# Performance work log

Measured on AMD Instinct MI355X. Metric: run time of the kernel, lower is better.

## Reference

```python
import jax, jax.numpy as jnp
import numpy as np

COMMITMENT_COST = 0.25


def setup_inputs() -> dict:
    key = jax.random.key(0)
    k1, k2 = jax.random.split(key)
    z_e = jax.random.normal(k1, (8, 2048, 768), dtype=jnp.float32)
    # torch init is uniform(-1/K, 1/K); scale is irrelevant for correctness,
    # but match it for realism.
    K = 8192
    embedding = jax.random.uniform(k2, (K, 768), dtype=jnp.float32,
                                   minval=-1.0 / K, maxval=1.0 / K)
    return {"z_e": z_e, "embedding": embedding}


def reference(z_e, embedding):
    """VectorQuantizer.forward (eval mode: no EMA side effects).

    Returns (quantized_st, indices, loss) exactly as the torch module.
    """
    B, S, D = z_e.shape
    flat = z_e.reshape(-1, D)  # [N, D]
    distances = (jnp.sum(flat * flat, axis=1, keepdims=True)
                 + jnp.sum(embedding * embedding, axis=1)
                 - 2.0 * flat @ embedding.T)
    indices = jnp.argmin(distances, axis=1)          # [N]
    quantized = embedding[indices].reshape(B, S, D)  # codebook lookup
    indices = indices.reshape(B, S)
    # commitment loss: mse(stop_grad(quantized), z_e)
    e_latent_loss = jnp.mean((jax.lax.stop_gradient(quantized) - z_e) ** 2)
    loss = COMMITMENT_COST * e_latent_loss
    # straight-through estimator
    quantized_st = z_e + jax.lax.stop_gradient(quantized - z_e)
    return quantized_st, indices, loss
```

## Files before the change

### kernel.cpp

```cpp
#include <hip/hip_runtime.h>
#include <cfloat>

#define NROWS 16384
#define DIM   768
#define KC    8192
#define MARGIN 2.5e-4f
#define NBLK_EMIT (NROWS / 4)

#define BM 256
#define BN 256
#define BK 32
#define NKT (DIM / BK)
#define NCB (KC / BN)

#define NBLK_ZCVT (NROWS / 4)
#define NBLK_ECVT (KC * DIM / 8 / 256)

typedef unsigned short ushort_t;
typedef __attribute__((ext_vector_type(8))) short short8v;
typedef __attribute__((ext_vector_type(4))) float f32x4;

__device__ __forceinline__ ushort_t f2bf(float f) {
  unsigned u = __float_as_uint(f);
  return (ushort_t)((u + 0x7FFFu + ((u >> 16) & 1u)) >> 16);
}

__device__ __forceinline__ void gload_lds16(const void* g, void* l) {
  using GP = const __attribute__((address_space(1))) void*;
  using LP = __attribute__((address_space(3))) void*;
  GP gp = (GP)(unsigned long long)(uintptr_t)g;
  LP lp = (LP)(unsigned)(uintptr_t)l;
  __builtin_amdgcn_global_load_lds(gp, lp, 16, 0, 0);
}

__global__ __launch_bounds__(256)
void cvt_all_kernel(const float* __restrict__ z, ushort_t* __restrict__ zh,
                    float* __restrict__ x2, const float* __restrict__ emb,
                    ushort_t* __restrict__ eh) {
#pragma clang fp contract(off)
  if (blockIdx.x < NBLK_ZCVT) {
    const int w    = threadIdx.x >> 6;
    const int lane = threadIdx.x & 63;
    const int n    = blockIdx.x * 4 + w;
    const float* zr = z + (size_t)n * DIM;

    {
      const float4* zg = (const float4*)zr;
      uint2* zo = (uint2*)(zh + (size_t)n * DIM);
      #pragma unroll
      for (int i = 0; i < 3; ++i) {
        const float4 f = zg[lane + 64 * i];
        uint2 o;
        o.x = (unsigned)f2bf(f.x) | ((unsigned)f2bf(f.y) << 16);
        o.y = (unsigned)f2bf(f.z) | ((unsigned)f2bf(f.w) << 16);
        zo[lane + 64 * i] = o;
      }
    }

    const int chunk = lane >> 3;
    const int j     = lane & 7;
    const float* p  = zr + chunk * 96 + j;
    float v0 = p[0];
    float r  = v0 * v0;
    #pragma unroll
    for (int k = 1; k < 12; ++k) {
      const float v  = p[8 * k];
      const float sq = v * v;
      r = r + sq;
    }
    r = r + __shfl_xor(r, 1);
    r = r + __shfl_xor(r, 2);
    r = r + __shfl_xor(r, 4);
    r = r + __shfl_xor(r, 8);
    r = r + __shfl_xor(r, 16);
    r = r + __shfl_xor(r, 32);
    if (lane == 0) x2[n] = r;
  } else {
    const int i = (blockIdx.x - NBLK_ZCVT) * 256 + threadIdx.x;
    const float4* s4 = (const float4*)emb;
    const float4 f0 = s4[2 * i], f1 = s4[2 * i + 1];
    uint4 o;
    o.x = (unsigned)f2bf(f0.x) | ((unsigned)f2bf(f0.y) << 16);
    o.y = (unsigned)f2bf(f0.z) | ((unsigned)f2bf(f0.w) << 16);
    o.z = (unsigned)f2bf(f1.x) | ((unsigned)f2bf(f1.y) << 16);
    o.w = (unsigned)f2bf(f1.z) | ((unsigned)f2bf(f1.w) << 16);
    ((uint4*)eh)[i] = o;
  }
}

__global__ __launch_bounds__(512, 2)
void gemm5(const ushort_t* __restrict__ zh, const ushort_t* __restrict__ eh,
           float4* __restrict__ subtop) {
  __shared__ __align__(16) ushort_t Ash[3][BM * BK];
  __shared__ __align__(16) ushort_t Bsh[3][BN * BK];
  __shared__ float4 ltop[BM][4];

  const int t    = threadIdx.x;
  const int w    = t >> 6, lane = t & 63;
  const int wr   = w >> 2;
  const int wcn  = w & 3;
  const int row0 = blockIdx.y * BM;
  const int col0 = blockIdx.x * BN;

  const int srow  = w * 32 + (lane >> 2);
  const int sslot = lane & 3;
  const ushort_t* zsA[2];
  const ushort_t* esB[2];
  #pragma unroll
  for (int q = 0; q < 2; ++q) {
    const int r = srow + q * 16;
    const int j = sslot ^ ((r >> 1) & 3);
    zsA[q] = zh + (size_t)(row0 + r) * DIM + j * 8;
    esB[q] = eh + (size_t)(col0 + r) * DIM + j * 8;
  }

#define STAGE_A_S(ktv, SLOT) do {                                         \
    _Pragma("unroll")                                                     \
    for (int q = 0; q < 2; ++q)                                           \
      gload_lds16(zsA[q] + (ktv) * 32, &Ash[SLOT][w * 1024 + q * 512]);   \
  } while (0)
#define STAGE_B_S(ktv, SLOT) do {                                         \
    _Pragma("unroll")                                                     \
    for (int q = 0; q < 2; ++q)                                           \
      gload_lds16(esB[q] + (ktv) * 32, &Bsh[SLOT][w * 1024 + q * 512]);   \
  } while (0)

  f32x4 acc[8][4];
  #pragma unroll
  for (int m = 0; m < 8; ++m)
    #pragma unroll
    for (int n = 0; n < 4; ++n) acc[m][n] = (f32x4){0.f, 0.f, 0.f, 0.f};

  STAGE_A_S(0, 0); STAGE_B_S(0, 0);
  STAGE_A_S(1, 1); STAGE_B_S(1, 1);
  asm volatile("s_waitcnt vmcnt(4)" ::: "memory");
  __builtin_amdgcn_s_barrier();
  __builtin_amdgcn_sched_barrier(0);

#define TILE_STEP(ktv, RB, RS) do {                                           \
    short8v bfr[4], afr[8];                                                   \
      \
    _Pragma("unroll")                                                         \
    for (int n = 0; n < 4; ++n) {                                             \
      const int c  = wcn * 64 + n * 16 + (lane & 15);                         \
      const int sl = (lane >> 4) ^ ((c >> 1) & 3);                            \
      bfr[n] = *(const short8v*)&Bsh[RB][c * 32 + sl * 8];                    \
    }                                                                         \
    _Pragma("unroll")                                                         \
    for (int m = 0; m < 8; ++m) {                                             \
      const int r  = wr * 128 + m * 16 + (lane & 15);                         \
      const int sl = (lane >> 4) ^ ((r >> 1) & 3);                            \
      afr[m] = *(const short8v*)&Ash[RB][r * 32 + sl * 8];                    \
    }                                                                         \
    if ((ktv) + 2 < NKT) { STAGE_A_S((ktv) + 2, RS); STAGE_B_S((ktv) + 2, RS); } \
    _Pragma("unroll")                                                         \
    for (int m = 0; m < 8; ++m)                                               \
      _Pragma("unroll")                                                       \
      for (int n = 0; n < 4; ++n)                                             \
        acc[m][n] = __builtin_amdgcn_mfma_f32_16x16x32_bf16(afr[m], bfr[n],   \
                                                            acc[m][n], 0, 0, 0); \
       \
    asm volatile("s_waitcnt lgkmcnt(0)" ::: "memory");                        \
    if ((ktv) < NKT - 2) asm volatile("s_waitcnt vmcnt(4)" ::: "memory");     \
    else                 asm volatile("s_waitcnt vmcnt(0)" ::: "memory");     \
    __builtin_amdgcn_s_barrier();                                             \
    asm volatile("" ::: "memory");                                            \
    __builtin_amdgcn_sched_barrier(0);                                        \
  } while (0)

  #pragma unroll 1
  for (int u = 0; u < NKT / 3; ++u) {
    const int kt = u * 3;
    TILE_STEP(kt + 0, 0, 2);
    TILE_STEP(kt + 1, 1, 0);
    TILE_STEP(kt + 2, 2, 1);
  }
#undef TILE_STEP
#undef STAGE_A_S
#undef STAGE_B_S

  __syncthreads();
  #pragma unroll
  for (int m = 0; m < 8; ++m) {
    #pragma unroll
    for (int reg = 0; reg < 4; ++reg) {
      float v1 = FLT_MAX, v2 = FLT_MAX; int i1 = 0, i2 = 0;
      #pragma unroll
      for (int n = 0; n < 4; ++n) {
        const float v = -2.0f * acc[m][n][reg];
        const int   c = col0 + wcn * 64 + n * 16 + (lane & 15);
        if (v < v1)      { v2 = v1; i2 = i1; v1 = v; i1 = c; }
        else if (v < v2) { v2 = v; i2 = c; }
      }
      #pragma unroll
      for (int off = 1; off < 16; off <<= 1) {
        const float ov1 = __shfl_xor(v1, off); const int oi1 = __shfl_xor(i1, off);
        const float ov2 = __shfl_xor(v2, off); const int oi2 = __shfl_xor(i2, off);
        if (ov1 < v1) {
          const float nv2 = (v1 < ov2) ? v1 : ov2;
          const int   ni2 = (v1 < ov2) ? i1 : oi2;
          v1 = ov1; i1 = oi1; v2 = nv2; i2 = ni2;
        } else if (ov1 < v2) { v2 = ov1; i2 = oi1; }
      }
      const int rloc = wr * 128 + m * 16 + (lane >> 4) * 4 + reg;
      if ((lane & 15) == 0)
        ltop[rloc][wcn] = make_float4(v1, __int_as_float(i1), v2, __int_as_float(i2));
    }
  }
  __syncthreads();
  if (t < BM) {
    float v1 = FLT_MAX, v2 = FLT_MAX; int i1 = 0x7fffffff, i2 = 0x7fffffff;
    #pragma unroll
    for (int g = 0; g < 4; ++g) {
      const float4 P = ltop[t][g];
      const float pv1 = P.x; const int pi1 = __float_as_int(P.y);
      const float pv2 = P.z; const int pi2 = __float_as_int(P.w);
      if (pv1 < v1)      { v2 = v1; i2 = i1; v1 = pv1; i1 = pi1; }
      else if (pv1 < v2) { v2 = pv1; i2 = pi1; }
      if (pv2 < v1)      { v2 = v1; i2 = i1; v1 = pv2; i1 = pi2; }
      else if (pv2 < v2) { v2 = pv2; i2 = pi2; }
    }
    subtop[(size_t)(row0 + t) * NCB + blockIdx.x] =
        make_float4(v1, __int_as_float(i1), v2, __int_as_float(i2));
  }
}

__global__ __launch_bounds__(256)
void selemit_k(const float* __restrict__ z, const float* __restrict__ emb,
               const float* __restrict__ x2, const float4* __restrict__ subtop,
               float* __restrict__ out, double* __restrict__ partials) {
  __shared__ float zbuf[4][DIM];
  __shared__ float ebufA[4][DIM];
  __shared__ float ebufB[4][DIM];
  __shared__ double wsum[4];

  const int w    = threadIdx.x >> 6;
  const int lane = threadIdx.x & 63;
  const int n    = blockIdx.x * 4 + w;

  float v1 = FLT_MAX, v2 = FLT_MAX;
  int i1 = 0x7fffffff;
  if (lane < NCB) {
    const float4 e = subtop[(size_t)n * NCB + lane];
    v1 = e.x; i1 = __float_as_int(e.y);
    v2 = e.z;
  }

  float rowmin = v1;
  #pragma unroll
  for (int off = 32; off; off >>= 1) rowmin = fminf(rowmin, __shfl_xor(rowmin, off));
  const float thr = rowmin + MARGIN;

  const unsigned long long mA = __ballot(v1 <= thr);
  const unsigned long long mB = __ballot(v2 <= thr);

  int winner;
  if (mB == 0 && __popcll(mA) == 1) {
    winner = __shfl(i1, __builtin_ctzll(mA));
  } else {
    const float x2n = x2[n];
    {
      const float4* zg = (const float4*)(z + (size_t)n * DIM);
      float4* zl = (float4*)zbuf[w];
      #pragma unroll
      for (int i = 0; i < 3; ++i) zl[lane + 64 * i] = zg[lane + 64 * i];
    }
    float bd = FLT_MAX; int bc = 0x7fffffff;

    unsigned long long mS = mA & ~mB;
    while (mS) {
      const int s0 = __builtin_ctzll(mS); mS &= mS - 1;
      int s1 = -1;
      if (mS) { s1 = __builtin_ctzll(mS); mS &= mS - 1; }
      const int ca = __shfl(i1, s0);
      const int cb = (s1 >= 0) ? __shfl(i1, s1) : -1;
      {
        const float4* eg = (const float4*)(emb + (size_t)ca * DIM);
        float4* el = (float4*)ebufA[w];
        #pragma unroll
        for (int i = 0; i < 3; ++i) el[lane + 64 * i] = eg[lane + 64 * i];
      }
      if (cb >= 0) {
        const float4* eg = (const float4*)(emb + (size_t)cb * DIM);
        float4* el = (float4*)ebufB[w];
        #pragma unroll
        for (int i = 0; i < 3; ++i) el[lane + 64 * i] = eg[lane + 64 * i];
      }
      asm volatile("s_waitcnt lgkmcnt(0)" ::: "memory");
      const float4* zl4 = (const float4*)zbuf[w];
      const float4* la4 = (const float4*)ebufA[w];
      const float4* lb4 = (const float4*)ebufB[w];
      float da = 0.f, db = 0.f;
      #pragma unroll 8
      for (int kq = 0; kq < DIM / 4; ++kq) {
        const float4 zz = zl4[kq];
        const float4 aa = la4[kq];
        const float4 bb = lb4[kq];
        da = fmaf(zz.x, aa.x, da); db = fmaf(zz.x, bb.x, db);
        da = fmaf(zz.y, aa.y, da); db = fmaf(zz.y, bb.y, db);
        da = fmaf(zz.z, aa.z, da); db = fmaf(zz.z, bb.z, db);
        da = fmaf(zz.w, aa.w, da); db = fmaf(zz.w, bb.w, db);
      }
      const float sa = x2n - 2.0f * da;
      if (sa < bd || (sa == bd && ca < bc)) { bd = sa; bc = ca; }
      if (cb >= 0) {
        const float sb = x2n - 2.0f * db;
        if (sb < bd || (sb == bd && cb < bc)) { bd = sb; bc = cb; }
      }
    }

    unsigned long long m = mB;
    if (m) {
      const float* zr = z + (size_t)n * DIM;
      float bdL = FLT_MAX; int bcL = 0x7fffffff;
      while (m) {
        const int s = __builtin_ctzll(m); m &= m - 1;
        const int c0 = s * BN + lane;
        const float* p0 = emb + (size_t)c0 * DIM;
        const float* p1 = p0 + (size_t)64 * DIM;
        const float* p2 = p0 + (size_t)128 * DIM;
        const float* p3 = p0 + (size_t)192 * DIM;
        float d0 = 0.f, d1 = 0.f, d2 = 0.f, d3 = 0.f;
        #pragma unroll 4
        for (int k = 0; k < DIM; ++k) {
          const float zk = zr[k];
          d0 = fmaf(zk, p0[k], d0);
          d1 = fmaf(zk, p1[k], d1);
          d2 = fmaf(zk, p2[k], d2);
          d3 = fmaf(zk, p3[k], d3);
        }
        const float s0 = x2n - 2.0f * d0;
        const float s1 = x2n - 2.0f * d1;
        const float s2 = x2n - 2.0f * d2;
        const float s3 = x2n - 2.0f * d3;
        if (s0 < bdL || (s0 == bdL && c0 < bcL))       { bdL = s0; bcL = c0; }
        if (s1 < bdL || (s1 == bdL && c0 + 64 < bcL))  { bdL = s1; bcL = c0 + 64; }
        if (s2 < bdL || (s2 == bdL && c0 + 128 < bcL)) { bdL = s2; bcL = c0 + 128; }
        if (s3 < bdL || (s3 == bdL && c0 + 192 < bcL)) { bdL = s3; bcL = c0 + 192; }
      }
      #pragma unroll
      for (int off = 32; off; off >>= 1) {
        const float ov = __shfl_xor(bdL, off);
        const int   oc = __shfl_xor(bcL, off);
        if (ov < bdL || (ov == bdL && oc < bcL)) { bdL = ov; bcL = oc; }
      }
      if (bdL < bd || (bdL == bd && bcL < bc)) { bd = bdL; bc = bcL; }
    }
    winner = bc;
  }

  const float4* zr4 = (const float4*)(z + (size_t)n * DIM);
  const float4* er4 = (const float4*)(emb + (size_t)winner * DIM);
  float4* outr = (float4*)(out + (size_t)n * DIM);
  double lsum = 0.0;
  #pragma unroll
  for (int i = 0; i < 3; ++i) {
    const int idx = lane + 64 * i;
    const float4 zz = zr4[idx];
    const float4 qq = er4[idx];
    float4 o;
    o.x = zz.x + (qq.x - zz.x); o.y = zz.y + (qq.y - zz.y);
    o.z = zz.z + (qq.z - zz.z); o.w = zz.w + (qq.w - zz.w);
    outr[idx] = o;
    const float dx = qq.x - zz.x, dy = qq.y - zz.y;
    const float dz = qq.z - zz.z, dw = qq.w - zz.w;
    lsum = fma((double)dx, (double)dx, lsum);
    lsum = fma((double)dy, (double)dy, lsum);
    lsum = fma((double)dz, (double)dz, lsum);
    lsum = fma((double)dw, (double)dw, lsum);
  }
  #pragma unroll
  for (int off = 32; off; off >>= 1) lsum += __shfl_xor(lsum, off);
  if (lane == 0) {
    out[(size_t)NROWS * DIM + n] = (float)winner;
    wsum[w] = lsum;
  }
  __syncthreads();
  if (threadIdx.x == 0)
    partials[blockIdx.x] = ((wsum[0] + wsum[1]) + (wsum[2] + wsum[3]));
}

__global__ __launch_bounds__(256)
void fin_kernel(const double* __restrict__ partials, float* __restrict__ out) {
  __shared__ double red[256];
  const int t = threadIdx.x;
  double s = 0.0;
  #pragma unroll
  for (int i = 0; i < NBLK_EMIT / 256; ++i) s += partials[t * (NBLK_EMIT / 256) + i];
  red[t] = s;
  __syncthreads();
  for (int off = 128; off; off >>= 1) {
    if (t < off) red[t] += red[t + off];
    __syncthreads();
  }
  if (t == 0)
    out[(size_t)NROWS * DIM + NROWS] =
        (float)(0.25 * red[0] / (double)((size_t)NROWS * DIM));
}

extern "C" void kernel_launch(void* const* d_in, const int* in_sizes, int n_in,
                              void* d_out, int out_size, void* d_ws, size_t ws_size,
                              hipStream_t stream) {
  const float* z   = (const float*)d_in[0];
  const float* emb = (const float*)d_in[1];
  float* out = (float*)d_out;
  char*  ws  = (char*)d_ws;

  double*   partials = (double*)ws;
  float*    x2       = (float*)(ws + 32768);
  ushort_t* zh       = (ushort_t*)(ws + 163840);
  ushort_t* eh       = (ushort_t*)(ws + 25329664);
  float4*   subtop   = (float4*)(ws + 37912576);

  cvt_all_kernel<<<NBLK_ZCVT + NBLK_ECVT, 256, 0, stream>>>(z, zh, x2, emb, eh);
  gemm5<<<dim3(KC / BN, NROWS / BM), 512, 0, stream>>>(zh, eh, subtop);
  selemit_k<<<NROWS / 4, 256, 0, stream>>>(z, emb, x2, subtop, out, partials);
  fin_kernel<<<1, 256, 0, stream>>>(partials, out);
}
```

Baseline: 462.3 us.

## Shrink GEMM column tile to 128 and alias top-2 scratch onto LDS

Halves the codebook tile width (BN 256→128) so each 8-wave block computes a 256x128 tile with 4x4 MFMA accumulators per wave instead of 8x4. The aim is lower register pressure, higher occupancy and more blocks in the grid. The per-row top-2 scratch now reuses the A-tile LDS buffer instead of a separate array. The refine kernel is adjusted to 64 column-block candidates per row, which fills every lane. The cost is less operand reuse per loaded tile and twice as much subtop data written and read.

```diff
diff --git a/kernel.cpp b/kernel.cpp
--- a/kernel.cpp
+++ b/kernel.cpp
@@ -8,7 +8,7 @@
 #define NBLK_EMIT (NROWS / 4)
 
 #define BM 256
-#define BN 256
+#define BN 128
 #define BK 32
 #define NKT (DIM / BK)
 #define NCB (KC / BN)
@@ -88,80 +88,67 @@
   }
 }
 
-__global__ __launch_bounds__(512, 2)
-void gemm5(const ushort_t* __restrict__ zh, const ushort_t* __restrict__ eh,
+__global__ __launch_bounds__(512)
+void gemm6(const ushort_t* __restrict__ zh, const ushort_t* __restrict__ eh,
            float4* __restrict__ subtop) {
   __shared__ __align__(16) ushort_t Ash[3][BM * BK];
   __shared__ __align__(16) ushort_t Bsh[3][BN * BK];
-  __shared__ float4 ltop[BM][4];
 
   const int t    = threadIdx.x;
   const int w    = t >> 6, lane = t & 63;
-  const int wr   = w >> 2;
-  const int wcn  = w & 3;
+  const int wr   = w >> 1;
+  const int wcn  = w & 1;
   const int row0 = blockIdx.y * BM;
   const int col0 = blockIdx.x * BN;
-
-  const int srow  = w * 32 + (lane >> 2);
-  const int sslot = lane & 3;
-  const ushort_t* zsA[2];
-  const ushort_t* esB[2];
-  #pragma unroll
-  for (int q = 0; q < 2; ++q) {
-    const int r = srow + q * 16;
-    const int j = sslot ^ ((r >> 1) & 3);
-    zsA[q] = zh + (size_t)(row0 + r) * DIM + j * 8;
-    esB[q] = eh + (size_t)(col0 + r) * DIM + j * 8;
-  }
-
-#define STAGE_A_S(ktv, SLOT) do {                                         \
-    _Pragma("unroll")                                                     \
-    for (int q = 0; q < 2; ++q)                                           \
-      gload_lds16(zsA[q] + (ktv) * 32, &Ash[SLOT][w * 1024 + q * 512]);   \
+  const int l15  = lane & 15;
+  const int qa8  = ((lane >> 4) ^ ((lane >> 1) & 3)) * 8;
+
+  const int rS = t >> 2;
+  const int jS = ((t & 3) ^ ((rS >> 1) & 3)) * 8;
+  const ushort_t* srcA0 = zh + (size_t)(row0 + rS) * DIM + jS;
+  const ushort_t* srcA1 = srcA0 + (size_t)128 * DIM;
+  const ushort_t* srcB0 = eh + (size_t)(col0 + rS) * DIM + jS;
+
+#define STG(ktv, SLOT) do {                                               \
+    gload_lds16(srcA0 + (ktv) * 32, &Ash[SLOT][w * 512]);                 \
+    gload_lds16(srcA1 + (ktv) * 32, &Ash[SLOT][4096 + w * 512]);          \
+    gload_lds16(srcB0 + (ktv) * 32, &Bsh[SLOT][w * 512]);                 \
   } while (0)
-#define STAGE_B_S(ktv, SLOT) do {                                         \
-    _Pragma("unroll")                                                     \
-    for (int q = 0; q < 2; ++q)                                           \
-      gload_lds16(esB[q] + (ktv) * 32, &Bsh[SLOT][w * 1024 + q * 512]);   \
-  } while (0)
-
-  f32x4 acc[8][4];
-  #pragma unroll
-  for (int m = 0; m < 8; ++m)
+
+  f32x4 acc[4][4];
+  #pragma unroll
+  for (int m = 0; m < 4; ++m)
     #pragma unroll
     for (int n = 0; n < 4; ++n) acc[m][n] = (f32x4){0.f, 0.f, 0.f, 0.f};
 
-  STAGE_A_S(0, 0); STAGE_B_S(0, 0);
-  STAGE_A_S(1, 1); STAGE_B_S(1, 1);
-  asm volatile("s_waitcnt vmcnt(4)" ::: "memory");
+  STG(0, 0);
+  STG(1, 1);
+  asm volatile("s_waitcnt vmcnt(3)" ::: "memory");
   __builtin_amdgcn_s_barrier();
   __builtin_amdgcn_sched_barrier(0);
 
 #define TILE_STEP(ktv, RB, RS) do {                                           \
-    short8v bfr[4], afr[8];                                                   \
-      \
+    short8v bfr[4], afr[4];                                                   \
     _Pragma("unroll")                                                         \
     for (int n = 0; n < 4; ++n) {                                             \
-      const int c  = wcn * 64 + n * 16 + (lane & 15);                         \
-      const int sl = (lane >> 4) ^ ((c >> 1) & 3);                            \
-      bfr[n] = *(const short8v*)&Bsh[RB][c * 32 + sl * 8];                    \
+      const int c = wcn * 64 + n * 16 + l15;                                  \
+      bfr[n] = *(const short8v*)&Bsh[RB][c * 32 + qa8];                       \
     }                                                                         \
     _Pragma("unroll")                                                         \
-    for (int m = 0; m < 8; ++m) {                                             \
-      const int r  = wr * 128 + m * 16 + (lane & 15);                         \
-      const int sl = (lane >> 4) ^ ((r >> 1) & 3);                            \
-      afr[m] = *(const short8v*)&Ash[RB][r * 32 + sl * 8];                    \
+    for (int m = 0; m < 4; ++m) {                                             \
+      const int r = wr * 64 + m * 16 + l15;                                   \
+      afr[m] = *(const short8v*)&Ash[RB][r * 32 + qa8];                       \
     }                                                                         \
-    if ((ktv) + 2 < NKT) { STAGE_A_S((ktv) + 2, RS); STAGE_B_S((ktv) + 2, RS); } \
+    if ((ktv) + 2 < NKT) STG((ktv) + 2, RS);                                  \
     _Pragma("unroll")                                                         \
-    for (int m = 0; m < 8; ++m)                                               \
+    for (int m = 0; m < 4; ++m)                                               \
       _Pragma("unroll")                                                       \
       for (int n = 0; n < 4; ++n)                                             \
         acc[m][n] = __builtin_amdgcn_mfma_f32_16x16x32_bf16(afr[m], bfr[n],   \
                                                             acc[m][n], 0, 0, 0); \
        \
     asm volatile("s_waitcnt lgkmcnt(0)" ::: "memory");                        \
-    if ((ktv) < NKT - 2) asm volatile("s_waitcnt vmcnt(4)" ::: "memory");     \
+    if ((ktv) < NKT - 2) asm volatile("s_waitcnt vmcnt(3)" ::: "memory");     \
     else                 asm volatile("s_waitcnt vmcnt(0)" ::: "memory");     \
     __builtin_amdgcn_s_barrier();                                             \
     asm volatile("" ::: "memory");                                            \
@@ -176,19 +163,20 @@
     TILE_STEP(kt + 2, 2, 1);
   }
 #undef TILE_STEP
-#undef STAGE_A_S
-#undef STAGE_B_S
+#undef STG
 
   __syncthreads();
-  #pragma unroll
-  for (int m = 0; m < 8; ++m) {
+  float4* ltop = (float4*)(void*)&Ash[0][0];
+
+  #pragma unroll
+  for (int m = 0; m < 4; ++m) {
     #pragma unroll
     for (int reg = 0; reg < 4; ++reg) {
       float v1 = FLT_MAX, v2 = FLT_MAX; int i1 = 0, i2 = 0;
       #pragma unroll
       for (int n = 0; n < 4; ++n) {
         const float v = -2.0f * acc[m][n][reg];
-        const int   c = col0 + wcn * 64 + n * 16 + (lane & 15);
+        const int   c = col0 + wcn * 64 + n * 16 + l15;
         if (v < v1)      { v2 = v1; i2 = i1; v1 = v; i1 = c; }
         else if (v < v2) { v2 = v; i2 = c; }
       }
@@ -202,17 +190,18 @@
           v1 = ov1; i1 = oi1; v2 = nv2; i2 = ni2;
         } else if (ov1 < v2) { v2 = ov1; i2 = oi1; }
       }
-      const int rloc = wr * 128 + m * 16 + (lane >> 4) * 4 + reg;
-      if ((lane & 15) == 0)
-        ltop[rloc][wcn] = make_float4(v1, __int_as_float(i1), v2, __int_as_float(i2));
+      const int rloc = wr * 64 + m * 16 + (lane >> 4) * 4 + reg;
+      if (l15 == 0)
+        ltop[rloc * 2 + wcn] = make_float4(v1, __int_as_float(i1),
+                                           v2, __int_as_float(i2));
     }
   }
   __syncthreads();
   if (t < BM) {
     float v1 = FLT_MAX, v2 = FLT_MAX; int i1 = 0x7fffffff, i2 = 0x7fffffff;
     #pragma unroll
-    for (int g = 0; g < 4; ++g) {
-      const float4 P = ltop[t][g];
+    for (int g = 0; g < 2; ++g) {
+      const float4 P = ltop[t * 2 + g];
       const float pv1 = P.x; const int pi1 = __float_as_int(P.y);
       const float pv2 = P.z; const int pi2 = __float_as_int(P.w);
       if (pv1 < v1)      { v2 = v1; i2 = i1; v1 = pv1; i1 = pi1; }
@@ -240,7 +229,7 @@
 
   float v1 = FLT_MAX, v2 = FLT_MAX;
   int i1 = 0x7fffffff;
-  if (lane < NCB) {
+  {
     const float4 e = subtop[(size_t)n * NCB + lane];
     v1 = e.x; i1 = __float_as_int(e.y);
     v2 = e.z;
@@ -318,25 +307,17 @@
         const int c0 = s * BN + lane;
         const float* p0 = emb + (size_t)c0 * DIM;
         const float* p1 = p0 + (size_t)64 * DIM;
-        const float* p2 = p0 + (size_t)128 * DIM;
-        const float* p3 = p0 + (size_t)192 * DIM;
-        float d0 = 0.f, d1 = 0.f, d2 = 0.f, d3 = 0.f;
-        #pragma unroll 4
+        float d0 = 0.f, d1 = 0.f;
+        #pragma unroll 8
         for (int k = 0; k < DIM; ++k) {
           const float zk = zr[k];
           d0 = fmaf(zk, p0[k], d0);
           d1 = fmaf(zk, p1[k], d1);
-          d2 = fmaf(zk, p2[k], d2);
-          d3 = fmaf(zk, p3[k], d3);
         }
         const float s0 = x2n - 2.0f * d0;
         const float s1 = x2n - 2.0f * d1;
-        const float s2 = x2n - 2.0f * d2;
-        const float s3 = x2n - 2.0f * d3;
-        if (s0 < bdL || (s0 == bdL && c0 < bcL))       { bdL = s0; bcL = c0; }
-        if (s1 < bdL || (s1 == bdL && c0 + 64 < bcL))  { bdL = s1; bcL = c0 + 64; }
-        if (s2 < bdL || (s2 == bdL && c0 + 128 < bcL)) { bdL = s2; bcL = c0 + 128; }
-        if (s3 < bdL || (s3 == bdL && c0 + 192 < bcL)) { bdL = s3; bcL = c0 + 192; }
+        if (s0 < bdL || (s0 == bdL && c0 < bcL))      { bdL = s0; bcL = c0; }
+        if (s1 < bdL || (s1 == bdL && c0 + 64 < bcL)) { bdL = s1; bcL = c0 + 64; }
       }
       #pragma unroll
       for (int off = 32; off; off >>= 1) {
@@ -413,7 +394,7 @@
   float4*   subtop   = (float4*)(ws + 37912576);
 
   cvt_all_kernel<<<NBLK_ZCVT + NBLK_ECVT, 256, 0, stream>>>(z, zh, x2, emb, eh);
-  gemm5<<<dim3(KC / BN, NROWS / BM), 512, 0, stream>>>(zh, eh, subtop);
+  gemm6<<<dim3(KC / BN, NROWS / BM), 512, 0, stream>>>(zh, eh, subtop);
   selemit_k<<<NROWS / 4, 256, 0, stream>>>(z, emb, x2, subtop, out, partials);
   fin_kernel<<<1, 256, 0, stream>>>(partials, out);
 }
```

New measurement: 450.7 us. 1.03x faster.
